# Kernel tuning notes

Measured on AMD Instinct MI355X. Metric: run time of the kernel, lower is better.

Reference implementation:

```python
import jax, jax.numpy as jnp
import numpy as np

BIG = 1e10  # sentinel for masked min/max (squared distances are << BIG)


def _boundary_mask(img, num_classes):
    """Union over classes v>0 of pixels adjacent (4-neighborhood) to a class change.
    Matches extract_boundaries: final (boundaries > 0) is the union of per-class masks."""
    b = jnp.zeros(img.shape, dtype=bool)
    for v in range(1, num_classes):
        m = img == v
        dv = m[:-1, :] != m[1:, :]   # vertical neighbor differs
        dh = m[:, :-1] != m[:, 1:]   # horizontal neighbor differs
        b = b | jnp.pad(dv, ((0, 1), (0, 0))) | jnp.pad(dv, ((1, 0), (0, 0)))
        b = b | jnp.pad(dh, ((0, 0), (0, 1))) | jnp.pad(dh, ((0, 0), (1, 0)))
    return b


def _pairwise_sqdist(H, W):
    ii, jj = jnp.meshgrid(jnp.arange(H), jnp.arange(W), indexing='ij')
    coords = jnp.stack([ii.ravel(), jj.ravel()], axis=1).astype(jnp.float32)  # [N,2]
    sq = jnp.sum(coords * coords, axis=1)
    d2 = sq[:, None] + sq[None, :] - 2.0 * (coords @ coords.T)  # [N,N]
    return jnp.maximum(d2, 0.0)


def _hausdorff(m1, m2, d2):
    # directed(A->B) on SQUARED distances (sqrt is monotone, applied once at the end)
    min_to2 = jnp.min(jnp.where(m2[None, :], d2, BIG), axis=1)   # [N] nearest pt in set2
    fwd = jnp.max(jnp.where(m1, min_to2, -BIG))
    min_to1 = jnp.min(jnp.where(m1[None, :], d2, BIG), axis=1)
    bwd = jnp.max(jnp.where(m2, min_to1, -BIG))
    return jnp.sqrt(jnp.maximum(jnp.maximum(fwd, bwd), 0.0))


def setup_inputs() -> dict:
    key = jax.random.key(0)
    k1, k2 = jax.random.split(key)
    B, C, H, W = 4, 4, 96, 96
    output = jax.random.normal(k1, (B, C, H, W), dtype=jnp.float32)
    target = jax.random.randint(k2, (B, H, W), 0, C, dtype=jnp.int32)
    return {"output": output, "target": target}


def reference(output, target):
    B, C, H, W = output.shape
    pred = jnp.argmax(output, axis=1)  # [B,H,W]
    mask_pred = jax.vmap(lambda im: _boundary_mask(im, C))(pred).reshape(B, -1)
    mask_tgt = jax.vmap(lambda im: _boundary_mask(im, C))(target).reshape(B, -1)
    d2 = _pairwise_sqdist(H, W)  # shared [N,N] grid distances
    dists = jax.lax.map(lambda mm: _hausdorff(mm[0], mm[1], d2), (mask_pred, mask_tgt))
    return dists.mean()
```

## Files before the change

### kernel.cpp

```cpp
#include <hip/hip_runtime.h>
#include <math.h>

#define BB 4
#define CC 4
#define HH 96
#define WW 96
#define NN (HH * WW)
#define WPR (WW / 4)
#define NW (NN / 4)
#define BIGF 1e10f
#define QROWS (HH / 4)

__global__ __launch_bounds__(1024) void k_fused(const float* __restrict__ out,
                                                const int* __restrict__ tgt,
                                                float* __restrict__ partial) {
    __shared__ __align__(16) unsigned char smem[64512];
    unsigned char* predL  = smem;
    unsigned char* tgtL   = smem + 9216;
    float* gq             = (float*)smem;
    unsigned char* maskE  = smem + 36864;
    unsigned char* maskO  = smem + 46080;
    unsigned int* colbits = (unsigned int*)(smem + 55296);
    float* red            = (float*)(smem + 57216);

    const int blk = blockIdx.x;
    const int q = blk & 3;
    const int e = (blk >> 2) & 1;
    const int b = blk >> 3;
    const int tid = threadIdx.x;

    const float* obase = out + (size_t)b * CC * NN;
    const int* tbase = tgt + b * NN;
    for (int w = tid; w < NW; w += 1024) {
        int p = w * 4;
        float4 c0 = *(const float4*)(obase + p);
        float4 c1 = *(const float4*)(obase + NN + p);
        float4 c2 = *(const float4*)(obase + 2 * NN + p);
        float4 c3 = *(const float4*)(obase + 3 * NN + p);
        unsigned int pk = 0;
        {
            float bv = c0.x; int bc = 0;
            if (c1.x > bv) { bv = c1.x; bc = 1; }
            if (c2.x > bv) { bv = c2.x; bc = 2; }
            if (c3.x > bv) { bv = c3.x; bc = 3; }
            pk |= (unsigned int)bc;
        }
        {
            float bv = c0.y; int bc = 0;
            if (c1.y > bv) { bv = c1.y; bc = 1; }
            if (c2.y > bv) { bv = c2.y; bc = 2; }
            if (c3.y > bv) { bv = c3.y; bc = 3; }
            pk |= (unsigned int)bc << 8;
        }
        {
            float bv = c0.z; int bc = 0;
            if (c1.z > bv) { bv = c1.z; bc = 1; }
            if (c2.z > bv) { bv = c2.z; bc = 2; }
            if (c3.z > bv) { bv = c3.z; bc = 3; }
            pk |= (unsigned int)bc << 16;
        }
        {
            float bv = c0.w; int bc = 0;
            if (c1.w > bv) { bv = c1.w; bc = 1; }
            if (c2.w > bv) { bv = c2.w; bc = 2; }
            if (c3.w > bv) { bv = c3.w; bc = 3; }
            pk |= (unsigned int)bc << 24;
        }
        ((unsigned int*)predL)[w] = pk;
        int4 tv = *(const int4*)(tbase + p);
        ((unsigned int*)tgtL)[w] =
            (tv.x & 0xFF) | ((tv.y & 0xFF) << 8) | ((tv.z & 0xFF) << 16) | ((tv.w & 0xFF) << 24);
    }
    __syncthreads();

    const unsigned int* pw = (const unsigned int*)predL;
    const unsigned int* tw = (const unsigned int*)tgtL;
    for (int w = tid; w < NW; w += 1024) {
        int i = w / WPR;
        int jw = w - i * WPR;
        unsigned int mP, mT;
        #pragma unroll
        for (int s = 0; s < 2; ++s) {
            const unsigned int* src = s ? tw : pw;
            unsigned int c = src[w];
            unsigned int diff = 0;
            if (i > 0)      diff |= c ^ src[w - WPR];
            if (i < HH - 1) diff |= c ^ src[w + WPR];
            unsigned int l = (c << 8) | (jw > 0 ? (src[w - 1] >> 24) : (c & 0xFFu));
            diff |= c ^ l;
            unsigned int r = (c >> 8) | (jw < WPR - 1 ? (src[w + 1] << 24) : (c & 0xFF000000u));
            diff |= c ^ r;
            unsigned int y = (((diff & 0x7F7F7F7Fu) + 0x7F7F7F7Fu) | diff) & 0x80808080u;
            unsigned int m01 = (y >> 7);
            if (s) mT = m01; else mP = m01;
        }
        ((unsigned int*)maskE)[w] = e ? mT : mP;
        ((unsigned int*)maskO)[w] = e ? mP : mT;
    }
    __syncthreads();

    if (tid < 96 * 3) {
        int j = tid / 3, w = tid - j * 3;
        const unsigned char* colp = &maskE[w * 32 * WW + j];
        unsigned int bits = 0;
        #pragma unroll
        for (int r = 0; r < 32; ++r) bits |= ((unsigned int)colp[r * WW]) << r;
        colbits[j * 5 + w] = bits;
    }
    __syncthreads();

    const int pix0 = q * QROWS * WW;
    for (int p4 = tid; p4 < QROWS * WW; p4 += 1024) {
        int p = pix0 + p4;
        int i = p / WW;
        int j = p - i * WW;
        unsigned int w0 = colbits[j * 5 + 0];
        unsigned int w1 = colbits[j * 5 + 1];
        unsigned int hi = colbits[j * 5 + 2];
        unsigned long long lo = (unsigned long long)w0 | ((unsigned long long)w1 << 32);
        int up = 1 << 20, dn = 1 << 20;
        if (i < 64) {
            unsigned long long mu = lo & (~0ull >> (63 - i));
            if (mu) up = i - (63 - __clzll(mu));
            unsigned long long md = lo >> i;
            if (md) dn = __ffsll(md) - 1;
            else if (hi) dn = (64 - i) + (__ffs(hi) - 1);
        } else {
            int ih = i - 64;
            unsigned int mu = hi & (0xFFFFFFFFu >> (31 - ih));
            if (mu) up = ih - (31 - __clz(mu));
            else if (lo) up = i - (63 - __clzll(lo));
            unsigned int md = hi >> ih;
            if (md) dn = __ffs(md) - 1;
        }
        int d = (up < dn) ? up : dn;
        gq[p] = (d < HH) ? (float)(d * d) : BIGF;
    }
    __syncthreads();

    float m = -BIGF;
    for (int p4 = tid; p4 < QROWS * WW; p4 += 1024) {
        int p = pix0 + p4;
        int i = p / WW;
        int j = p - i * WW;
        const float* grow = &gq[i * WW];
        float best = grow[j];
        for (int o = 1; o < WW; ++o) {
            float o2 = (float)(o * o);
            if (o2 >= best) break;
            int jl = j - o, jr = j + o;
            if (jl >= 0)  best = fminf(best, grow[jl] + o2);
            if (jr < WW)  best = fminf(best, grow[jr] + o2);
        }
        if (maskO[p]) m = fmaxf(m, best);
    }
    #pragma unroll
    for (int off = 32; off > 0; off >>= 1) m = fmaxf(m, __shfl_down(m, off));
    const int wid = tid >> 6, lid = tid & 63;
    if (lid == 0) red[wid] = m;
    __syncthreads();
    if (tid == 0) {
        float mm = red[0];
        #pragma unroll
        for (int w = 1; w < 16; ++w) mm = fmaxf(mm, red[w]);
        partial[blk] = mm;
    }
}

__global__ void k_fin(const float* __restrict__ partial, float* __restrict__ outv) {
    if (threadIdx.x == 0) {
        float s = 0.0f;
        #pragma unroll
        for (int b = 0; b < BB; ++b) {
            float bwd = -BIGF, fwd = -BIGF;
            #pragma unroll
            for (int qq = 0; qq < 4; ++qq) {
                bwd = fmaxf(bwd, partial[b * 8 + qq]);
                fwd = fmaxf(fwd, partial[b * 8 + 4 + qq]);
            }
            s += sqrtf(fmaxf(fmaxf(fwd, bwd), 0.0f));
        }
        outv[0] = s * 0.25f;
    }
}

extern "C" void kernel_launch(void* const* d_in, const int* in_sizes, int n_in,
                              void* d_out, int out_size, void* d_ws, size_t ws_size,
                              hipStream_t stream) {
    const float* output = (const float*)d_in[0];
    const int* target   = (const int*)d_in[1];
    float* outv         = (float*)d_out;
    float* partial      = (float*)d_ws;

    k_fused<<<32, 1024, 0, stream>>>(output, target, partial);
    k_fin<<<1, 64, 0, stream>>>(partial, outv);
}
```

Baseline: 61.47 us.

## Split blocks into row octants and batch argmax loads per thread

The grid doubles from 32 to 64 blocks, each covering one eighth of the rows instead of a quarter, to spread work over more compute units. The argmax prologue is unrolled so each thread issues all three of its float4 iterations' loads up front, which raises memory-level parallelism. The row-min scan now skips non-boundary pixels early instead of computing and then discarding them. In exchange, each block still redundantly recomputes the full-image argmax, masks and column bits, so that duplicated prologue work also doubles.

New measurement: 61.35 us. No clear change (-0.2%).

```diff
diff --git a/kernel.cpp b/kernel.cpp
--- a/kernel.cpp
+++ b/kernel.cpp
@@ -9,7 +9,7 @@
 #define WPR (WW / 4)
 #define NW (NN / 4)
 #define BIGF 1e10f
-#define QROWS (HH / 4)
+#define OROWS (HH / 8)
 
 __global__ __launch_bounds__(1024) void k_fused(const float* __restrict__ out,
                                                 const int* __restrict__ tgt,
@@ -24,52 +24,60 @@
     float* red            = (float*)(smem + 57216);
 
     const int blk = blockIdx.x;
-    const int q = blk & 3;
-    const int e = (blk >> 2) & 1;
-    const int b = blk >> 3;
+    const int oct = blk & 7;
+    const int e = (blk >> 3) & 1;
+    const int b = blk >> 4;
     const int tid = threadIdx.x;
 
     const float* obase = out + (size_t)b * CC * NN;
     const int* tbase = tgt + b * NN;
-    for (int w = tid; w < NW; w += 1024) {
-        int p = w * 4;
-        float4 c0 = *(const float4*)(obase + p);
-        float4 c1 = *(const float4*)(obase + NN + p);
-        float4 c2 = *(const float4*)(obase + 2 * NN + p);
-        float4 c3 = *(const float4*)(obase + 3 * NN + p);
-        unsigned int pk = 0;
-        {
-            float bv = c0.x; int bc = 0;
-            if (c1.x > bv) { bv = c1.x; bc = 1; }
-            if (c2.x > bv) { bv = c2.x; bc = 2; }
-            if (c3.x > bv) { bv = c3.x; bc = 3; }
-            pk |= (unsigned int)bc;
-        }
-        {
-            float bv = c0.y; int bc = 0;
-            if (c1.y > bv) { bv = c1.y; bc = 1; }
-            if (c2.y > bv) { bv = c2.y; bc = 2; }
-            if (c3.y > bv) { bv = c3.y; bc = 3; }
-            pk |= (unsigned int)bc << 8;
-        }
-        {
-            float bv = c0.z; int bc = 0;
-            if (c1.z > bv) { bv = c1.z; bc = 1; }
-            if (c2.z > bv) { bv = c2.z; bc = 2; }
-            if (c3.z > bv) { bv = c3.z; bc = 3; }
-            pk |= (unsigned int)bc << 16;
-        }
-        {
-            float bv = c0.w; int bc = 0;
-            if (c1.w > bv) { bv = c1.w; bc = 1; }
-            if (c2.w > bv) { bv = c2.w; bc = 2; }
-            if (c3.w > bv) { bv = c3.w; bc = 3; }
-            pk |= (unsigned int)bc << 24;
-        }
-        ((unsigned int*)predL)[w] = pk;
-        int4 tv = *(const int4*)(tbase + p);
-        ((unsigned int*)tgtL)[w] =
-            (tv.x & 0xFF) | ((tv.y & 0xFF) << 8) | ((tv.z & 0xFF) << 16) | ((tv.w & 0xFF) << 24);
+    {
+        const int w0 = tid, w1 = tid + 1024, w2 = tid + 2048;
+        const bool has2 = (tid < NW - 2048);
+        const int p0 = w0 * 4, p1 = w1 * 4, p2 = has2 ? w2 * 4 : 0;
+
+        float4 a0 = *(const float4*)(obase + p0);
+        float4 a1 = *(const float4*)(obase + NN + p0);
+        float4 a2 = *(const float4*)(obase + 2 * NN + p0);
+        float4 a3 = *(const float4*)(obase + 3 * NN + p0);
+        float4 b0 = *(const float4*)(obase + p1);
+        float4 b1 = *(const float4*)(obase + NN + p1);
+        float4 b2 = *(const float4*)(obase + 2 * NN + p1);
+        float4 b3 = *(const float4*)(obase + 3 * NN + p1);
+        float4 c0 = *(const float4*)(obase + p2);
+        float4 c1 = *(const float4*)(obase + NN + p2);
+        float4 c2 = *(const float4*)(obase + 2 * NN + p2);
+        float4 c3 = *(const float4*)(obase + 3 * NN + p2);
+        int4 t0 = *(const int4*)(tbase + p0);
+        int4 t1 = *(const int4*)(tbase + p1);
+        int4 t2 = *(const int4*)(tbase + p2);
+
+        #define AMAX4(r0, r1, r2, r3, sh, pk) {            \
+            float bv = (r0); unsigned int bc = 0;          \
+            if ((r1) > bv) { bv = (r1); bc = 1; }          \
+            if ((r2) > bv) { bv = (r2); bc = 2; }          \
+            if ((r3) > bv) { bv = (r3); bc = 3; }          \
+            pk |= bc << (sh); }
+        unsigned int pk0 = 0, pk1 = 0, pk2 = 0;
+        AMAX4(a0.x, a1.x, a2.x, a3.x, 0,  pk0) AMAX4(a0.y, a1.y, a2.y, a3.y, 8,  pk0)
+        AMAX4(a0.z, a1.z, a2.z, a3.z, 16, pk0) AMAX4(a0.w, a1.w, a2.w, a3.w, 24, pk0)
+        AMAX4(b0.x, b1.x, b2.x, b3.x, 0,  pk1) AMAX4(b0.y, b1.y, b2.y, b3.y, 8,  pk1)
+        AMAX4(b0.z, b1.z, b2.z, b3.z, 16, pk1) AMAX4(b0.w, b1.w, b2.w, b3.w, 24, pk1)
+        AMAX4(c0.x, c1.x, c2.x, c3.x, 0,  pk2) AMAX4(c0.y, c1.y, c2.y, c3.y, 8,  pk2)
+        AMAX4(c0.z, c1.z, c2.z, c3.z, 16, pk2) AMAX4(c0.w, c1.w, c2.w, c3.w, 24, pk2)
+        #undef AMAX4
+
+        ((unsigned int*)predL)[w0] = pk0;
+        ((unsigned int*)predL)[w1] = pk1;
+        ((unsigned int*)tgtL)[w0] =
+            (t0.x & 0xFF) | ((t0.y & 0xFF) << 8) | ((t0.z & 0xFF) << 16) | ((t0.w & 0xFF) << 24);
+        ((unsigned int*)tgtL)[w1] =
+            (t1.x & 0xFF) | ((t1.y & 0xFF) << 8) | ((t1.z & 0xFF) << 16) | ((t1.w & 0xFF) << 24);
+        if (has2) {
+            ((unsigned int*)predL)[w2] = pk2;
+            ((unsigned int*)tgtL)[w2] =
+                (t2.x & 0xFF) | ((t2.y & 0xFF) << 8) | ((t2.z & 0xFF) << 16) | ((t2.w & 0xFF) << 24);
+        }
     }
     __syncthreads();
 
@@ -109,8 +117,8 @@
     }
     __syncthreads();
 
-    const int pix0 = q * QROWS * WW;
-    for (int p4 = tid; p4 < QROWS * WW; p4 += 1024) {
+    const int pix0 = oct * OROWS * WW;
+    for (int p4 = tid; p4 < OROWS * WW; p4 += 1024) {
         int p = pix0 + p4;
         int i = p / WW;
         int j = p - i * WW;
@@ -139,8 +147,9 @@
     __syncthreads();
 
     float m = -BIGF;
-    for (int p4 = tid; p4 < QROWS * WW; p4 += 1024) {
+    for (int p4 = tid; p4 < OROWS * WW; p4 += 1024) {
         int p = pix0 + p4;
+        if (!maskO[p]) continue;
         int i = p / WW;
         int j = p - i * WW;
         const float* grow = &gq[i * WW];
@@ -152,7 +161,7 @@
             if (jl >= 0)  best = fminf(best, grow[jl] + o2);
             if (jr < WW)  best = fminf(best, grow[jr] + o2);
         }
-        if (maskO[p]) m = fmaxf(m, best);
+        m = fmaxf(m, best);
     }
     #pragma unroll
     for (int off = 32; off > 0; off >>= 1) m = fmaxf(m, __shfl_down(m, off));
@@ -174,9 +183,9 @@
         for (int b = 0; b < BB; ++b) {
             float bwd = -BIGF, fwd = -BIGF;
             #pragma unroll
-            for (int qq = 0; qq < 4; ++qq) {
-                bwd = fmaxf(bwd, partial[b * 8 + qq]);
-                fwd = fmaxf(fwd, partial[b * 8 + 4 + qq]);
+            for (int oo = 0; oo < 8; ++oo) {
+                bwd = fmaxf(bwd, partial[b * 16 + oo]);
+                fwd = fmaxf(fwd, partial[b * 16 + 8 + oo]);
             }
             s += sqrtf(fmaxf(fmaxf(fwd, bwd), 0.0f));
         }
@@ -192,6 +201,6 @@
     float* outv         = (float*)d_out;
     float* partial      = (float*)d_ws;
 
-    k_fused<<<32, 1024, 0, stream>>>(output, target, partial);
+    k_fused<<<64, 1024, 0, stream>>>(output, target, partial);
     k_fin<<<1, 64, 0, stream>>>(partial, outv);
 }
```
